# Performance work log

Measured on AMD Instinct MI355X. Metric: run time of the kernel, lower is better.

## Reference

```python
import jax, jax.numpy as jnp
import numpy as np

T, IN, H, OUT = 4096, 2048, 2048, 1


def setup_inputs() -> dict:
    key = jax.random.key(0)
    ks = jax.random.split(key, 7)
    s = 0.02  # small init scale to keep gates in a sane range
    return {
        "x": jax.random.normal(ks[0], (T, 1, IN), dtype=jnp.float32),
        "W_ih": s * jax.random.normal(ks[1], (4 * H, IN), dtype=jnp.float32),
        "W_hh": s * jax.random.normal(ks[2], (4 * H, H), dtype=jnp.float32),
        "b_ih": s * jax.random.normal(ks[3], (4 * H,), dtype=jnp.float32),
        "b_hh": s * jax.random.normal(ks[4], (4 * H,), dtype=jnp.float32),
        "W_out": s * jax.random.normal(ks[5], (OUT, H), dtype=jnp.float32),
        "b_out": s * jax.random.normal(ks[6], (OUT,), dtype=jnp.float32),
    }


def reference(x, W_ih, W_hh, b_ih, b_hh, W_out, b_out):
    # Faithful LSTMCell loop (PyTorch gate order i, f, g, o) + per-step Linear.
    hidden = W_hh.shape[1]

    def step(carry, x_t):  # x_t: [1, IN]
        h, c = carry
        gates = x_t @ W_ih.T + b_ih + h @ W_hh.T + b_hh  # [1, 4H]
        i, f, g, o = jnp.split(gates, 4, axis=-1)
        i = jax.nn.sigmoid(i)
        f = jax.nn.sigmoid(f)
        g = jnp.tanh(g)
        o = jax.nn.sigmoid(o)
        c = f * c + i * g
        h = o * jnp.tanh(c)
        y = (h @ W_out.T + b_out)[0, 0]  # scalar, output_size == 1
        return (h, c), y

    h0 = jnp.zeros((1, hidden), dtype=x.dtype)
    c0 = jnp.zeros((1, hidden), dtype=x.dtype)
    _, res = jax.lax.scan(step, (h0, c0), x)
    return res  # [T]
```

## Files before the change

### kernel.cpp

```cpp
#include <hip/hip_runtime.h>

#define T_STEPS 4096
#define HD 2048
#define G4 8192
#define NWG 256
#define NTH 512
#define HSENT 0xFF80u
#define HSENT2 0xFF80FF80u

#define HB_OFF  131072
#define P_OFF   (131072 + 4096)
#define SMEM_BYTES (131072 + 4096 + 1024)

typedef __attribute__((ext_vector_type(8))) short bf16x8;
typedef __attribute__((ext_vector_type(4))) float f32x4;
typedef __attribute__((ext_vector_type(8))) unsigned short u16x8;
typedef __attribute__((ext_vector_type(2))) unsigned int u32x2;
typedef __attribute__((ext_vector_type(4))) unsigned int u32x4;

static __device__ __forceinline__ unsigned short f2bf(float f){
  union { float f; unsigned int u; } v; v.f = f;
  unsigned int r = (v.u + 0x7fffu + ((v.u >> 16) & 1u)) >> 16;
  return (unsigned short)r;
}
static __device__ __forceinline__ float bf2f(unsigned short s){
  union { unsigned int u; float f; } v; v.u = ((unsigned int)s) << 16;
  return v.f;
}

static __device__ __forceinline__ u32x2 ld2_uc(const unsigned int* p){
  u32x2 r;
  asm volatile("global_load_dwordx2 %0, %1, off sc0 sc1\n\ts_waitcnt vmcnt(0)"
               : "=v"(r) : "v"(p) : "memory");
  return r;
}
static __device__ __forceinline__ void st4_uc(unsigned int* p, u32x4 v){
  asm volatile("global_store_dwordx4 %0, %1, off sc0 sc1" :: "v"(p), "v"(v) : "memory");
}

__global__ void init_kernel(const float* __restrict__ b_ih, const float* __restrict__ b_hh,
                            float* __restrict__ bias, unsigned int* __restrict__ Hb32){
  int i = blockIdx.x*blockDim.x + threadIdx.x;
  int stride = gridDim.x*blockDim.x;
  const int HB_U32 = (T_STEPS+1)*HD/2;
  const int NTOT = G4 + HB_U32;
  for (int idx = i; idx < NTOT; idx += stride){
    if (idx < G4) bias[idx] = b_ih[idx] + b_hh[idx];
    else {
      int j = idx - G4;
      Hb32[j] = (j < HD/2) ? 0u : HSENT2;
    }
  }
}

__global__ __launch_bounds__(256) void gemm_xp(const float* __restrict__ X,
                                               const float* __restrict__ W,
                                               const float* __restrict__ bias,
                                               unsigned short* __restrict__ XP){
  __shared__ __align__(16) unsigned short As[128][40];
  __shared__ __align__(16) unsigned short Bs[128][40];
  const int tid = threadIdx.x;
  const int bx = blockIdx.x & 63;
  const int by = blockIdx.x >> 6;
  const int row0 = by*128, col0 = bx*128;
  const int l = tid & 63, w = tid >> 6;
  const int wrow = (w>>1)*64, wcol = (w&1)*64;
  const int lr = l & 15, lk = l >> 4;

  f32x4 acc[4][4];
  #pragma unroll
  for (int mi=0; mi<4; mi++)
    #pragma unroll
    for (int ni=0; ni<4; ni++)
      acc[mi][ni] = (f32x4){0.f,0.f,0.f,0.f};

  const int sr = tid >> 1;
  const int sh = (tid & 1) * 16;
  const float* xb = X + (size_t)(row0+sr)*2048 + sh;
  const float* wb = W + (size_t)(col0+sr)*2048 + sh;

  for (int k0 = 0; k0 < 2048; k0 += 32){
    __syncthreads();
    u16x8 va[2], vb[2];
    #pragma unroll
    for (int q=0; q<2; q++){
      float4 u = *(const float4*)(xb + k0 + q*8);
      float4 v = *(const float4*)(xb + k0 + q*8 + 4);
      u16x8 t;
      t[0]=f2bf(u.x); t[1]=f2bf(u.y); t[2]=f2bf(u.z); t[3]=f2bf(u.w);
      t[4]=f2bf(v.x); t[5]=f2bf(v.y); t[6]=f2bf(v.z); t[7]=f2bf(v.w);
      va[q]=t;
      float4 p = *(const float4*)(wb + k0 + q*8);
      float4 r = *(const float4*)(wb + k0 + q*8 + 4);
      u16x8 s;
      s[0]=f2bf(p.x); s[1]=f2bf(p.y); s[2]=f2bf(p.z); s[3]=f2bf(p.w);
      s[4]=f2bf(r.x); s[5]=f2bf(r.y); s[6]=f2bf(r.z); s[7]=f2bf(r.w);
      vb[q]=s;
    }
    *(u16x8*)&As[sr][sh]   = va[0];
    *(u16x8*)&As[sr][sh+8] = va[1];
    *(u16x8*)&Bs[sr][sh]   = vb[0];
    *(u16x8*)&Bs[sr][sh+8] = vb[1];
    __syncthreads();

    bf16x8 af[4], bfr[4];
    #pragma unroll
    for (int mi=0; mi<4; mi++) af[mi]  = *(const bf16x8*)&As[wrow+mi*16+lr][lk*8];
    #pragma unroll
    for (int ni=0; ni<4; ni++) bfr[ni] = *(const bf16x8*)&Bs[wcol+ni*16+lr][lk*8];
    #pragma unroll
    for (int mi=0; mi<4; mi++)
      #pragma unroll
      for (int ni=0; ni<4; ni++)
        acc[mi][ni] = __builtin_amdgcn_mfma_f32_16x16x32_bf16(af[mi], bfr[ni], acc[mi][ni], 0,0,0);
  }

  #pragma unroll
  for (int ni=0; ni<4; ni++){
    const int jc = col0 + wcol + ni*16 + lr;
    const float bv = bias[jc];
    #pragma unroll
    for (int mi=0; mi<4; mi++){
      const int tr0 = row0 + wrow + mi*16 + lk*4;
      #pragma unroll
      for (int r=0; r<4; r++)
        XP[(size_t)(tr0+r)*G4 + jc] = f2bf(acc[mi][ni][r] + bv);
    }
  }
}

__global__ __launch_bounds__(NTH, 1) void recur(const unsigned short* __restrict__ XP,
                                                const float* __restrict__ Whh,
                                                unsigned short* __restrict__ Hbuf){
  extern __shared__ char smem[];
  float* part = (float*)(smem + P_OFF);
  char*  hb   = smem + HB_OFF;
  const int g = blockIdx.x;
  const int tid = threadIdx.x;
  const int l = tid & 63, w = tid >> 6;

  #pragma unroll
  for (int n=0; n<2; n++)
    #pragma unroll
    for (int kt=0; kt<8; kt++){
      const int rr = n*16 + (l & 15);
      const size_t jrow = (size_t)(rr>>3)*HD + (size_t)g*8 + (rr&7);
      const int k = w*256 + kt*32 + (l>>4)*8;
      const float* wp = Whh + jrow*HD + k;
      float4 fa = *(const float4*)wp;
      float4 fb = *(const float4*)(wp + 4);
      uint4 pk;
      pk.x = ((unsigned)f2bf(fa.y)<<16) | f2bf(fa.x);
      pk.y = ((unsigned)f2bf(fa.w)<<16) | f2bf(fa.z);
      pk.z = ((unsigned)f2bf(fb.y)<<16) | f2bf(fb.x);
      pk.w = ((unsigned)f2bf(fb.w)<<16) | f2bf(fb.z);
      *(uint4*)(smem + (size_t)(((w*16 + n*8 + kt)*64 + l)*16)) = pk;
    }
  __syncthreads();

  float c_reg = 0.f;

  for (int t=0; t<T_STEPS; ++t){
    float xpv0=0.f, xpv1=0.f, xpv2=0.f, xpv3=0.f;
    if (tid < 8){
      const unsigned short* xp = XP + (size_t)t*G4 + (size_t)g*8 + tid;
      xpv0 = bf2f(xp[0]);
      xpv1 = bf2f(xp[HD]);
      xpv2 = bf2f(xp[2*HD]);
      xpv3 = bf2f(xp[3*HD]);
    }
    bf16x8 bfr0[8], bfr1[8];
    #pragma unroll
    for (int kt=0; kt<8; kt++){
      bfr0[kt] = *(const bf16x8*)(smem + (size_t)(((w*16 +     kt)*64 + l)*16));
      bfr1[kt] = *(const bf16x8*)(smem + (size_t)(((w*16 + 8 + kt)*64 + l)*16));
    }

    u32x2 hv;
    {
      const unsigned int* hp = (const unsigned int*)(Hbuf + (size_t)t*HD) + tid*2;
      do { hv = ld2_uc(hp); }
      while ((hv[0] & 0xFFFFu) == HSENT || (hv[0] >> 16) == HSENT ||
             (hv[1] & 0xFFFFu) == HSENT || (hv[1] >> 16) == HSENT);
    }
    *(u32x2*)(hb + tid*8) = hv;
    __syncthreads();

    bf16x8 af[8];
    #pragma unroll
    for (int kt=0; kt<8; kt++)
      af[kt] = *(const bf16x8*)(hb + (w*512 + kt*64 + (l>>4)*16));

    f32x4 acc0 = (f32x4){0.f,0.f,0.f,0.f};
    f32x4 acc1 = (f32x4){0.f,0.f,0.f,0.f};
    #pragma unroll
    for (int kt=0; kt<8; kt++){
      acc0 = __builtin_amdgcn_mfma_f32_16x16x32_bf16(af[kt], bfr0[kt], acc0, 0,0,0);
      acc1 = __builtin_amdgcn_mfma_f32_16x16x32_bf16(af[kt], bfr1[kt], acc1, 0,0,0);
    }
    if (l < 16){
      part[w*32 + l]      = acc0[0];
      part[w*32 + 16 + l] = acc1[0];
    }
    __syncthreads();

    if (w == 0 && l < 32){
      float tot = 0.f;
      #pragma unroll
      for (int q=0; q<8; q++) tot += part[q*32 + l];
      float fg = __shfl_down(tot, 8, 64);
      float gg = __shfl_down(tot, 16, 64);
      float og = __shfl_down(tot, 24, 64);
      if (l < 8){
        float ipre = tot + xpv0;
        float fpre = fg  + xpv1;
        float gpre = gg  + xpv2;
        float opre = og  + xpv3;
        float iv = 1.f/(1.f + __expf(-ipre));
        float fv = 1.f/(1.f + __expf(-fpre));
        float e2 = __expf(-2.f*gpre);
        float gv = (1.f - e2)/(1.f + e2);
        float ov = 1.f/(1.f + __expf(-opre));
        c_reg = fv*c_reg + iv*gv;
        float e2c = __expf(-2.f*c_reg);
        float th = (1.f - e2c)/(1.f + e2c);
        unsigned v = f2bf(ov*th);
        unsigned p1 = (unsigned)__shfl_xor((int)v, 1, 64);
        unsigned d01 = (v & 0xFFFFu) | (p1 << 16);
        unsigned d23 = (unsigned)__shfl_xor((int)d01, 2, 64);
        unsigned d45 = (unsigned)__shfl_xor((int)d01, 4, 64);
        unsigned d67 = (unsigned)__shfl_xor((int)d23, 4, 64);
        if (l == 0){
          u32x4 pk = (u32x4){d01, d23, d45, d67};
          st4_uc((unsigned int*)(Hbuf + (size_t)(t+1)*HD + (size_t)g*8), pk);
        }
      }
    }
  }
}

__global__ __launch_bounds__(256) void out_gemv(const unsigned short* __restrict__ Hbuf,
                                                const float* __restrict__ Wout,
                                                const float* __restrict__ bout,
                                                float* __restrict__ y){
  const int t = blockIdx.x;
  const int tid = threadIdx.x;
  u16x8 hv = *(const u16x8*)(Hbuf + (size_t)(t+1)*HD + tid*8);
  float4 w0 = *(const float4*)(Wout + tid*8);
  float4 w1 = *(const float4*)(Wout + tid*8 + 4);
  float s = bf2f(hv[0])*w0.x + bf2f(hv[1])*w0.y + bf2f(hv[2])*w0.z + bf2f(hv[3])*w0.w
          + bf2f(hv[4])*w1.x + bf2f(hv[5])*w1.y + bf2f(hv[6])*w1.z + bf2f(hv[7])*w1.w;
  #pragma unroll
  for (int off=32; off; off>>=1) s += __shfl_xor(s, off, 64);
  __shared__ float ps[4];
  if ((tid & 63) == 0) ps[tid>>6] = s;
  __syncthreads();
  if (tid == 0) y[t] = ps[0]+ps[1]+ps[2]+ps[3] + bout[0];
}

extern "C" void kernel_launch(void* const* d_in, const int* in_sizes, int n_in,
                              void* d_out, int out_size, void* d_ws, size_t ws_size,
                              hipStream_t stream) {
  const float* x    = (const float*)d_in[0];
  const float* Wih  = (const float*)d_in[1];
  const float* Whh  = (const float*)d_in[2];
  const float* b_ih = (const float*)d_in[3];
  const float* b_hh = (const float*)d_in[4];
  const float* Wout = (const float*)d_in[5];
  const float* bout = (const float*)d_in[6];
  float* y = (float*)d_out;

  char* ws = (char*)d_ws;
  unsigned short* XP   = (unsigned short*)(ws);
  unsigned short* Hbuf = (unsigned short*)(ws + 67108864);
  float* bias          = (float*)(ws + 83890176);

  init_kernel<<<2048, 256, 0, stream>>>(b_ih, b_hh, bias, (unsigned int*)Hbuf);
  gemm_xp<<<2048, 256, 0, stream>>>(x, Wih, bias, XP);

  hipFuncSetAttribute((const void*)recur,
                      hipFuncAttributeMaxDynamicSharedMemorySize, SMEM_BYTES);
  void* args[] = {(void*)&XP, (void*)&Whh, (void*)&Hbuf};
  hipLaunchCooperativeKernel((void*)recur, dim3(NWG), dim3(NTH), args,
                             SMEM_BYTES, stream);

  out_gemv<<<T_STEPS, 256, 0, stream>>>(Hbuf, Wout, bout, y);
}
```

Before: 11.28 ms.

## Keep recurrent weights in registers and drop per-step barrier

```diff
diff --git a/kernel.cpp b/kernel.cpp
--- a/kernel.cpp
+++ b/kernel.cpp
@@ -5,12 +5,7 @@
 #define G4 8192
 #define NWG 256
 #define NTH 512
-#define HSENT 0xFF80u
 #define HSENT2 0xFF80FF80u
-
-#define HB_OFF  131072
-#define P_OFF   (131072 + 4096)
-#define SMEM_BYTES (131072 + 4096 + 1024)
 
 typedef __attribute__((ext_vector_type(8))) short bf16x8;
 typedef __attribute__((ext_vector_type(4))) float f32x4;
@@ -132,13 +127,14 @@
 __global__ __launch_bounds__(NTH, 1) void recur(const unsigned short* __restrict__ XP,
                                                 const float* __restrict__ Whh,
                                                 unsigned short* __restrict__ Hbuf){
-  extern __shared__ char smem[];
-  float* part = (float*)(smem + P_OFF);
-  char*  hb   = smem + HB_OFF;
+  __shared__ __align__(16) char hb[4096];
+  __shared__ float part[2][256];
   const int g = blockIdx.x;
   const int tid = threadIdx.x;
   const int l = tid & 63, w = tid >> 6;
-
+  if (w == 0) __builtin_amdgcn_s_setprio(1);
+
+  bf16x8 bw0[8], bw1[8];
   #pragma unroll
   for (int n=0; n<2; n++)
     #pragma unroll
@@ -154,60 +150,52 @@
       pk.y = ((unsigned)f2bf(fa.w)<<16) | f2bf(fa.z);
       pk.z = ((unsigned)f2bf(fb.y)<<16) | f2bf(fb.x);
       pk.w = ((unsigned)f2bf(fb.w)<<16) | f2bf(fb.z);
-      *(uint4*)(smem + (size_t)(((w*16 + n*8 + kt)*64 + l)*16)) = pk;
-    }
-  __syncthreads();
+      bf16x8 fr;
+      *(uint4*)&fr = pk;
+      asm volatile("" : "+v"(fr));
+      if (n == 0) bw0[kt] = fr; else bw1[kt] = fr;
+    }
 
   float c_reg = 0.f;
+  float xpv0=0.f, xpv1=0.f, xpv2=0.f, xpv3=0.f;
+  if (tid < 8){
+    const unsigned short* xp = XP + (size_t)g*8 + tid;
+    xpv0 = bf2f(xp[0]);
+    xpv1 = bf2f(xp[HD]);
+    xpv2 = bf2f(xp[2*HD]);
+    xpv3 = bf2f(xp[3*HD]);
+  }
 
   for (int t=0; t<T_STEPS; ++t){
-    float xpv0=0.f, xpv1=0.f, xpv2=0.f, xpv3=0.f;
-    if (tid < 8){
-      const unsigned short* xp = XP + (size_t)t*G4 + (size_t)g*8 + tid;
-      xpv0 = bf2f(xp[0]);
-      xpv1 = bf2f(xp[HD]);
-      xpv2 = bf2f(xp[2*HD]);
-      xpv3 = bf2f(xp[3*HD]);
-    }
-    bf16x8 bfr0[8], bfr1[8];
-    #pragma unroll
-    for (int kt=0; kt<8; kt++){
-      bfr0[kt] = *(const bf16x8*)(smem + (size_t)(((w*16 +     kt)*64 + l)*16));
-      bfr1[kt] = *(const bf16x8*)(smem + (size_t)(((w*16 + 8 + kt)*64 + l)*16));
-    }
-
     u32x2 hv;
     {
-      const unsigned int* hp = (const unsigned int*)(Hbuf + (size_t)t*HD) + tid*2;
+      const unsigned int* hp = (const unsigned int*)(Hbuf + (size_t)t*HD) + w*128 + l*2;
       do { hv = ld2_uc(hp); }
-      while ((hv[0] & 0xFFFFu) == HSENT || (hv[0] >> 16) == HSENT ||
-             (hv[1] & 0xFFFFu) == HSENT || (hv[1] >> 16) == HSENT);
-    }
-    *(u32x2*)(hb + tid*8) = hv;
-    __syncthreads();
-
+      while (hv[0] == HSENT2 || hv[1] == HSENT2);
+    }
+    *(u32x2*)(hb + w*512 + l*8) = hv;
     bf16x8 af[8];
     #pragma unroll
     for (int kt=0; kt<8; kt++)
-      af[kt] = *(const bf16x8*)(hb + (w*512 + kt*64 + (l>>4)*16));
+      af[kt] = *(const bf16x8*)(hb + w*512 + kt*64 + (l>>4)*16);
 
     f32x4 acc0 = (f32x4){0.f,0.f,0.f,0.f};
     f32x4 acc1 = (f32x4){0.f,0.f,0.f,0.f};
     #pragma unroll
     for (int kt=0; kt<8; kt++){
-      acc0 = __builtin_amdgcn_mfma_f32_16x16x32_bf16(af[kt], bfr0[kt], acc0, 0,0,0);
-      acc1 = __builtin_amdgcn_mfma_f32_16x16x32_bf16(af[kt], bfr1[kt], acc1, 0,0,0);
+      acc0 = __builtin_amdgcn_mfma_f32_16x16x32_bf16(af[kt], bw0[kt], acc0, 0,0,0);
+      acc1 = __builtin_amdgcn_mfma_f32_16x16x32_bf16(af[kt], bw1[kt], acc1, 0,0,0);
     }
     if (l < 16){
-      part[w*32 + l]      = acc0[0];
-      part[w*32 + 16 + l] = acc1[0];
+      part[t&1][w*32 + l]      = acc0[0];
+      part[t&1][w*32 + 16 + l] = acc1[0];
     }
     __syncthreads();
 
     if (w == 0 && l < 32){
       float tot = 0.f;
       #pragma unroll
-      for (int q=0; q<8; q++) tot += part[q*32 + l];
+      for (int q=0; q<8; q++) tot += part[t&1][q*32 + l];
       float fg = __shfl_down(tot, 8, 64);
       float gg = __shfl_down(tot, 16, 64);
       float og = __shfl_down(tot, 24, 64);
@@ -236,6 +224,14 @@
         }
       }
     }
+    if (tid < 8){
+      const int tn = (t+1 < T_STEPS) ? t+1 : t;
+      const unsigned short* xp = XP + (size_t)tn*G4 + (size_t)g*8 + tid;
+      xpv0 = bf2f(xp[0]);
+      xpv1 = bf2f(xp[HD]);
+      xpv2 = bf2f(xp[2*HD]);
+      xpv3 = bf2f(xp[3*HD]);
+    }
   }
 }
 
@@ -278,11 +274,8 @@
   init_kernel<<<2048, 256, 0, stream>>>(b_ih, b_hh, bias, (unsigned int*)Hbuf);
   gemm_xp<<<2048, 256, 0, stream>>>(x, Wih, bias, XP);
 
-  hipFuncSetAttribute((const void*)recur,
-                      hipFuncAttributeMaxDynamicSharedMemorySize, SMEM_BYTES);
   void* args[] = {(void*)&XP, (void*)&Whh, (void*)&Hbuf};
-  hipLaunchCooperativeKernel((void*)recur, dim3(NWG), dim3(NTH), args,
-                             SMEM_BYTES, stream);
+  hipLaunchCooperativeKernel((void*)recur, dim3(NWG), dim3(NTH), args, 0, stream);
 
   out_gemv<<<T_STEPS, 256, 0, stream>>>(Hbuf, Wout, bout, y);
 }
```

Result: no change. 11.14 ms (-1.3%).
